# Optimization experiments

Measured on AMD Instinct MI355X. Metric: run time of the kernel, lower is better.

The kernel has to match this reference:

```python
import jax, jax.numpy as jnp
import numpy as np

H = 1024          # en_hidden_size
NUM_LAYERS = 3
NUM_CLASS = 60
IN_SIZE = 150
EPS = 1e-5


def _gru_dir(x, w_ih, w_hh, b_ih, b_hh):
    """Single-direction GRU run forward in time. x: [N,T,in] -> [N,T,H].
    PyTorch GRU cell math."""
    gi = jnp.einsum('nti,gi->ntg', x, w_ih) + b_ih  # [N,T,3H] input projections

    def step(h, gi_t):
        gh = h @ w_hh.T + b_hh
        i_r, i_z, i_n = jnp.split(gi_t, 3, axis=-1)
        h_r, h_z, h_n = jnp.split(gh, 3, axis=-1)
        r = jax.nn.sigmoid(i_r + h_r)
        z = jax.nn.sigmoid(i_z + h_z)
        n = jnp.tanh(i_n + r * h_n)
        h_new = (1.0 - z) * n + z * h
        return h_new, h_new

    h0 = jnp.zeros((x.shape[0], H), dtype=x.dtype)
    _, ys = jax.lax.scan(step, h0, jnp.swapaxes(gi, 0, 1))  # ys: [T,N,H]
    return jnp.swapaxes(ys, 0, 1)


def _bigru_forward(x, bn_gamma, bn_beta,
                   w_ih_0, w_hh_0, b_ih_0, b_hh_0,
                   w_ih_1, w_hh_1, b_ih_1, b_hh_1,
                   w_ih_2, w_hh_2, b_ih_2, b_hh_2,
                   fc_w, fc_b):
    # BatchNorm1d (train mode): stats over (N,T) per channel, biased variance.
    mean = jnp.mean(x, axis=(0, 1), keepdims=True)
    var = jnp.mean(jnp.square(x - mean), axis=(0, 1), keepdims=True)
    h_in = (x - mean) * jax.lax.rsqrt(var + EPS) * bn_gamma + bn_beta

    # NOTE: the original advances the bidirectional GRU one timestep at a time
    # while carrying the hidden state, so BOTH directions run forward in time.
    layer_params = [(w_ih_0, w_hh_0, b_ih_0, b_hh_0),
                    (w_ih_1, w_hh_1, b_ih_1, b_hh_1),
                    (w_ih_2, w_hh_2, b_ih_2, b_hh_2)]
    for (w_ih, w_hh, b_ih, b_hh) in layer_params:
        outs = [_gru_dir(h_in, w_ih[d], w_hh[d], b_ih[d], b_hh[d]) for d in range(2)]
        h_in = jnp.concatenate(outs, axis=-1)  # [N,T,2H]

    encoder_hidden = h_in                      # [N,T,2H]
    hidden = encoder_hidden[:, -1, :]          # seq_len == T for every sample
    out = hidden @ fc_w.T + fc_b               # [N, num_class]
    return out, encoder_hidden


def setup_inputs() -> dict:
    key = jax.random.key(0)
    ks = jax.random.split(key, 32)
    N, T = 256, 64
    s = 1.0 / np.sqrt(H)
    inp = {}
    inp['x'] = jax.random.normal(ks[0], (N, T, IN_SIZE), dtype=jnp.float32)
    inp['bn_gamma'] = jnp.ones((IN_SIZE,), jnp.float32)
    inp['bn_beta'] = jnp.zeros((IN_SIZE,), jnp.float32)
    in_sizes = [IN_SIZE, 2 * H, 2 * H]
    ki = 1
    for l in range(NUM_LAYERS):
        inp[f'w_ih_{l}'] = jax.random.uniform(ks[ki], (2, 3 * H, in_sizes[l]), jnp.float32, -s, s); ki += 1
        inp[f'w_hh_{l}'] = jax.random.uniform(ks[ki], (2, 3 * H, H), jnp.float32, -s, s); ki += 1
        inp[f'b_ih_{l}'] = jax.random.uniform(ks[ki], (2, 3 * H), jnp.float32, -s, s); ki += 1
        inp[f'b_hh_{l}'] = jax.random.uniform(ks[ki], (2, 3 * H), jnp.float32, -s, s); ki += 1
    inp['fc_w'] = jax.random.uniform(ks[ki], (NUM_CLASS, 2 * H), jnp.float32, -s, s); ki += 1
    inp['fc_b'] = jax.random.uniform(ks[ki], (NUM_CLASS,), jnp.float32, -s, s)
    return inp


def reference(x, bn_gamma, bn_beta,
              w_ih_0, w_hh_0, b_ih_0, b_hh_0,
              w_ih_1, w_hh_1, b_ih_1, b_hh_1,
              w_ih_2, w_hh_2, b_ih_2, b_hh_2,
              fc_w, fc_b):
    return _bigru_forward(x, bn_gamma, bn_beta,
                          w_ih_0, w_hh_0, b_ih_0, b_hh_0,
                          w_ih_1, w_hh_1, b_ih_1, b_hh_1,
                          w_ih_2, w_hh_2, b_ih_2, b_hh_2,
                          fc_w, fc_b)
```

## Files before the change

### kernel.cpp

```cpp
#include <hip/hip_runtime.h>
#include <hip/hip_bf16.h>
#include <math.h>

#define HH    1024
#define TT    64
#define NBAT  256
#define G3    3072
#define IN0   150
#define IN0P  160
#define NCLS  60
#define ENC_W 2048

typedef float  f32x4 __attribute__((ext_vector_type(4)));
typedef short  s16x8 __attribute__((ext_vector_type(8)));

#define GLOAD16(gsrc, ldst) \
  __builtin_amdgcn_global_load_lds((const __attribute__((address_space(1))) unsigned int*)(gsrc), \
                                   (__attribute__((address_space(3))) unsigned int*)(ldst), 16, 0, 0)

static __device__ inline short f2bf(float f) {
    __hip_bfloat16 h = __float2bfloat16(f);
    return *(short*)&h;
}

__global__ void bigru_bn_stats(const float* __restrict__ x,
                               float* __restrict__ mean, float* __restrict__ istd) {
    int f = blockIdx.x;
    int tid = threadIdx.x;
    double s = 0.0, s2 = 0.0;
    for (int i = tid; i < NBAT * TT; i += blockDim.x) {
        float v = x[(size_t)i * IN0 + f];
        s += v; s2 += (double)v * v;
    }
    __shared__ double sh[256], sh2[256];
    sh[tid] = s; sh2[tid] = s2;
    __syncthreads();
    for (int off = 128; off > 0; off >>= 1) {
        if (tid < off) { sh[tid] += sh[tid + off]; sh2[tid] += sh2[tid + off]; }
        __syncthreads();
    }
    if (tid == 0) {
        double m = sh[0] / (NBAT * TT);
        double var = sh2[0] / (NBAT * TT) - m * m;
        mean[f] = (float)m;
        istd[f] = (float)(1.0 / sqrt(var + 1e-5));
    }
}

__global__ void bigru_bn_apply_bf16(const float* __restrict__ x,
                                    const float* __restrict__ mean, const float* __restrict__ istd,
                                    const float* __restrict__ gamma, const float* __restrict__ beta,
                                    short* __restrict__ xn) {
    int idx = blockIdx.x * blockDim.x + threadIdx.x;
    if (idx >= NBAT * TT * IN0P) return;
    int f = idx % IN0P;
    int r = idx / IN0P;
    float v = 0.f;
    if (f < IN0) v = (x[(size_t)r * IN0 + f] - mean[f]) * istd[f] * gamma[f] + beta[f];
    xn[idx] = f2bf(v);
}

__global__ void bigru_cvt_wih0(const float* __restrict__ src, short* __restrict__ dst) {
    int idx = blockIdx.x * blockDim.x + threadIdx.x;
    if (idx >= 2 * G3 * IN0P) return;
    int f = idx % IN0P;
    int r = idx / IN0P;
    float v = (f < IN0) ? src[(size_t)r * IN0 + f] : 0.f;
    dst[idx] = f2bf(v);
}

__global__ void bigru_cvt4(const float* __restrict__ src, short* __restrict__ dst, int n4) {
    int i = blockIdx.x * blockDim.x + threadIdx.x;
    if (i >= n4) return;
    float4 v = ((const float4*)src)[i];
    short4 o;
    o.x = f2bf(v.x); o.y = f2bf(v.y); o.z = f2bf(v.z); o.w = f2bf(v.w);
    ((short4*)dst)[i] = o;
}

__global__ __launch_bounds__(256)
void bigru_gi_gemm(const short* __restrict__ Abase, int ldA, int K,
                   const short* __restrict__ W,
                   const float* __restrict__ b_ih,
                   float* __restrict__ gi,
                   int t0, int Mchunk) {
    int d    = blockIdx.z;
    int col0 = blockIdx.x * 128;
    int row0 = blockIdx.y * 128;

    __shared__ short As[128][32];
    __shared__ short Bs[128][32];

    int tid  = threadIdx.x;
    int lane = tid & 63;
    int w    = tid >> 6;
    int wm   = w & 1, wn = w >> 1;

    f32x4 acc[4][4];
    #pragma unroll
    for (int i = 0; i < 4; ++i)
        #pragma unroll
        for (int j = 0; j < 4; ++j)
            acc[i][j] = (f32x4){0.f, 0.f, 0.f, 0.f};

    const short* Wd = W + (size_t)d * G3 * K;
    int sr = lane >> 2;
    int sc = (lane & 3) * 8;

    for (int k0 = 0; k0 < K; k0 += 32) {
        #pragma unroll
        for (int q = 0; q < 2; ++q) {
            int r  = w * 32 + q * 16 + sr;
            int gr = row0 + r;
            int tt = gr >> 8, n = gr & 255;
            const short* ga = Abase + (size_t)(n * TT + t0 + tt) * ldA + k0 + sc;
            GLOAD16(ga, &As[w * 32 + q * 16][0]);
            const short* gb = Wd + (size_t)(col0 + r) * K + k0 + sc;
            GLOAD16(gb, &Bs[w * 32 + q * 16][0]);
        }
        __syncthreads();

        int fr = lane & 15, fq = (lane >> 4) * 8;
        s16x8 a[4], b[4];
        #pragma unroll
        for (int i = 0; i < 4; ++i) a[i] = *(const s16x8*)&As[wm * 64 + i * 16 + fr][fq];
        #pragma unroll
        for (int j = 0; j < 4; ++j) b[j] = *(const s16x8*)&Bs[wn * 64 + j * 16 + fr][fq];
        #pragma unroll
        for (int i = 0; i < 4; ++i)
            #pragma unroll
            for (int j = 0; j < 4; ++j)
                acc[i][j] = __builtin_amdgcn_mfma_f32_16x16x32_bf16(a[i], b[j], acc[i][j], 0, 0, 0);
        __syncthreads();
    }

    int fr = lane & 15, quad = lane >> 4;
    #pragma unroll
    for (int j = 0; j < 4; ++j) {
        int c = col0 + wn * 64 + j * 16 + fr;
        float bias = b_ih[d * G3 + c];
        #pragma unroll
        for (int i = 0; i < 4; ++i) {
            #pragma unroll
            for (int reg = 0; reg < 4; ++reg) {
                int r = row0 + wm * 64 + i * 16 + quad * 4 + reg;
                gi[((size_t)d * Mchunk + r) * G3 + c] = acc[i][j][reg] + bias;
            }
        }
    }
}

__global__ __launch_bounds__(512, 1)
void bigru_steps_fused(const short* __restrict__ w_hh,
                       const float* __restrict__ b_hh,
                       const float* __restrict__ gi,
                       float* __restrict__ h,
                       short* __restrict__ hbf,
                       float* __restrict__ enc,
                       short* __restrict__ enc_bf,
                       unsigned int* __restrict__ bar,
                       int t0, int Tc, int Mchunk) {
    __shared__ short Ws[48 * 1024];
    __shared__ short As[8][4][512];

    int b   = blockIdx.x;
    int d   = b & 1;
    int mt  = (b >> 1) & 1;
    int ct  = b >> 2;
    int grp = b & 3;

    int tid  = threadIdx.x;
    int lane = tid & 63;
    int w    = tid >> 6;
    int fr   = lane & 15;
    int quad = lane >> 4;
    int sw   = fr & 7;

    int j0 = ct * 16;
    int row_base = mt * 128 + w * 16;
    int jcol = j0 + fr;

    const short* Wd = w_hh + (size_t)d * G3 * HH;

    #pragma unroll
    for (int q = 0; q < 12; ++q) {
        int c  = w * 12 + q;
        int rr = c >> 1, kh = c & 1;
        int g  = rr >> 4, jc = rr & 15;
        const short* src = Wd + (size_t)(g * HH + j0 + jc) * HH
                         + (size_t)(kh * 64 + (lane ^ (rr & 7))) * 8;
        GLOAD16(src, &Ws[rr * 1024 + kh * 512]);
    }

    int l0 = lane & 1, l1 = (lane >> 1) & 1, l2 = (lane >> 2) & 1;
    int l3 = (lane >> 3) & 1, l4 = (lane >> 4) & 1, l5 = (lane >> 5) & 1;
    int arow = (l2 ^ l4) | (l3 << 1) | (l4 << 2) | (l5 << 3);
    int akb  = (l0 ^ l2 ^ l4) | ((l1 ^ l3) << 1);
    size_t a_src_off = (size_t)(row_base + arow) * HH + (size_t)akb * 8;

    float hreg[4];
    #pragma unroll
    for (int r = 0; r < 4; ++r) {
        int n = row_base + quad * 4 + r;
        hreg[r] = h[((size_t)d * NBAT + n) * HH + jcol];
    }
    float bhr = b_hh[d * G3 + jcol];
    float bhz = b_hh[d * G3 + HH + jcol];
    float bhn = b_hh[d * G3 + 2 * HH + jcol];

    __syncthreads();

    float gir[4], giz[4], gin[4];
    {
        size_t gb0 = ((size_t)d * Mchunk) * G3 + jcol;
        #pragma unroll
        for (int r = 0; r < 4; ++r) {
            int n = row_base + quad * 4 + r;
            size_t gg = gb0 + (size_t)n * G3;
            gir[r] = gi[gg];
            giz[r] = gi[gg + HH];
            gin[r] = gi[gg + 2 * HH];
        }
    }

    for (int tt = 0; tt < Tc; ++tt) {
        int t = t0 + tt;
        const short* hb = hbf + ((size_t)((t & 1) * 2 + d)) * NBAT * HH;
        short*       ho = hbf + ((size_t)(((t + 1) & 1) * 2 + d)) * NBAT * HH;
        const short* asrc = hb + a_src_off;

        f32x4 acc[3];
        #pragma unroll
        for (int g = 0; g < 3; ++g) acc[g] = (f32x4){0.f, 0.f, 0.f, 0.f};

        #pragma unroll
        for (int c = 0; c < 3; ++c)
            GLOAD16(asrc + c * 32, &As[w][c][0]);

        int rd_off = (fr * 64 + quad * 16) ^ ((fr & 7) << 4);

        #pragma unroll
        for (int c = 0; c < 32; ++c) {
            if (c < 30)       asm volatile("s_waitcnt vmcnt(2)");
            else if (c == 30) asm volatile("s_waitcnt vmcnt(1)");
            else              asm volatile("s_waitcnt vmcnt(0)");
            __builtin_amdgcn_sched_barrier(0);
            s16x8 a = *(const s16x8*)((const char*)&As[w][c & 3][0] + rd_off);
            int ks = c * 4 + quad;
            #pragma unroll
            for (int g = 0; g < 3; ++g) {
                s16x8 bg = *(const s16x8*)&Ws[(g * 16 + fr) * 1024 + ((ks ^ sw) << 3)];
                acc[g] = __builtin_amdgcn_mfma_f32_16x16x32_bf16(a, bg, acc[g], 0, 0, 0);
            }
            __builtin_amdgcn_sched_barrier(0);
            if (c + 3 < 32)
                GLOAD16(asrc + (c + 3) * 32, &As[w][(c + 3) & 3][0]);
        }

        #pragma unroll
        for (int r = 0; r < 4; ++r) {
            int n = row_base + quad * 4 + r;
            float hrv = acc[0][r] + bhr;
            float hzv = acc[1][r] + bhz;
            float hnv = acc[2][r] + bhn;
            float rg = 1.f / (1.f + __expf(-(gir[r] + hrv)));
            float zg = 1.f / (1.f + __expf(-(giz[r] + hzv)));
            float ng = tanhf(gin[r] + rg * hnv);
            float hnew = (1.f - zg) * ng + zg * hreg[r];
            hreg[r] = hnew;
            ho[(size_t)n * HH + jcol] = f2bf(hnew);
            size_t eidx = ((size_t)n * TT + t) * ENC_W + (size_t)d * HH + jcol;
            if (enc_bf) enc_bf[eidx] = f2bf(hnew);
            if (enc)    enc[eidx]    = hnew;
        }

        if (tt == Tc - 1) {
            #pragma unroll
            for (int r = 0; r < 4; ++r) {
                int n = row_base + quad * 4 + r;
                h[((size_t)d * NBAT + n) * HH + jcol] = hreg[r];
            }
        } else {
            size_t gbn = ((size_t)d * Mchunk + (size_t)(tt + 1) * NBAT) * G3 + jcol;
            #pragma unroll
            for (int r = 0; r < 4; ++r) {
                int n = row_base + quad * 4 + r;
                size_t gg = gbn + (size_t)n * G3;
                gir[r] = gi[gg];
                giz[r] = gi[gg + HH];
                gin[r] = gi[gg + 2 * HH];
            }
            __syncthreads();
            if (w == 0) {
                unsigned int* fl = bar + (size_t)grp * 64 * 32;
                unsigned tgt = (unsigned)(tt + 1);
                if (lane == 0)
                    __hip_atomic_store(&fl[ct * 32], tgt,
                                       __ATOMIC_RELEASE, __HIP_MEMORY_SCOPE_AGENT);
                for (;;) {
                    unsigned v = __hip_atomic_load(&fl[lane * 32],
                                                   __ATOMIC_ACQUIRE, __HIP_MEMORY_SCOPE_AGENT);
                    if (__all(v >= tgt)) break;
                    __builtin_amdgcn_s_sleep(2);
                }
            }
            __syncthreads();
        }
    }
}

__global__ void bigru_fc(const float* __restrict__ enc, const float* __restrict__ fc_w,
                         const float* __restrict__ fc_b, float* __restrict__ out) {
    int n = blockIdx.x;
    int tid = threadIdx.x;
    __shared__ float hbuf[ENC_W];
    for (int k = tid; k < ENC_W; k += blockDim.x)
        hbuf[k] = enc[(size_t)n * TT * ENC_W + (size_t)(TT - 1) * ENC_W + k];
    __syncthreads();
    if (tid < NCLS) {
        float acc = fc_b[tid];
        for (int k = 0; k < ENC_W; ++k)
            acc += hbuf[k] * fc_w[(size_t)tid * ENC_W + k];
        out[(size_t)n * NCLS + tid] = acc;
    }
}

extern "C" void kernel_launch(void* const* d_in, const int* in_sizes, int n_in,
                              void* d_out, int out_size, void* d_ws, size_t ws_size,
                              hipStream_t stream) {
    const float* x        = (const float*)d_in[0];
    const float* bn_gamma = (const float*)d_in[1];
    const float* bn_beta  = (const float*)d_in[2];
    const float* w_ih[3]  = {(const float*)d_in[3], (const float*)d_in[7],  (const float*)d_in[11]};
    const float* w_hh[3]  = {(const float*)d_in[4], (const float*)d_in[8],  (const float*)d_in[12]};
    const float* b_ih[3]  = {(const float*)d_in[5], (const float*)d_in[9],  (const float*)d_in[13]};
    const float* b_hh[3]  = {(const float*)d_in[6], (const float*)d_in[10], (const float*)d_in[14]};
    const float* fc_w     = (const float*)d_in[15];
    const float* fc_b     = (const float*)d_in[16];

    float* out = (float*)d_out;
    float* enc = out + NBAT * NCLS;

    char* base = (char*)d_ws;
    size_t off = 0;
    auto alloc = [&](size_t bytes) {
        void* p = base + off;
        off += (bytes + 255) & ~(size_t)255;
        return p;
    };
    float* mean      = (float*)alloc(IN0 * 4);
    float* istd      = (float*)alloc(IN0 * 4);
    short* xn_bf     = (short*)alloc((size_t)NBAT * TT * IN0P * 2);
    short* wih0_bf   = (short*)alloc((size_t)2 * G3 * IN0P * 2);
    short* wih_bf    = (short*)alloc((size_t)2 * G3 * ENC_W * 2);
    short* whh_bf    = (short*)alloc((size_t)2 * G3 * HH * 2);
    float* h         = (float*)alloc((size_t)2 * NBAT * HH * 4);
    short* hbf       = (short*)alloc((size_t)2 * 2 * NBAT * HH * 2);
    short* enc_bf    = (short*)alloc((size_t)NBAT * TT * ENC_W * 2);
    unsigned int* bar = (unsigned int*)alloc((size_t)4 * 64 * 32 * sizeof(unsigned int));
    size_t fixed = off;

    int Tc = 1;
    for (int cand : {16, 8, 4, 2, 1}) {
        size_t gi_bytes = (size_t)2 * NBAT * cand * G3 * 4;
        if (fixed + gi_bytes + 1024 <= ws_size) { Tc = cand; break; }
    }
    float* gi = (float*)alloc((size_t)2 * NBAT * Tc * G3 * 4);
    int Mchunk = NBAT * Tc;

    bigru_bn_stats<<<IN0, 256, 0, stream>>>(x, mean, istd);
    bigru_bn_apply_bf16<<<(NBAT * TT * IN0P + 255) / 256, 256, 0, stream>>>(
        x, mean, istd, bn_gamma, bn_beta, xn_bf);

    bigru_cvt_wih0<<<(2 * G3 * IN0P + 255) / 256, 256, 0, stream>>>(w_ih[0], wih0_bf);

    for (int l = 0; l < 3; ++l) {
        if (l > 0) {
            int n4 = (2 * G3 * ENC_W) / 4;
            bigru_cvt4<<<(n4 + 255) / 256, 256, 0, stream>>>(w_ih[l], wih_bf, n4);
        }
        {
            int n4 = (2 * G3 * HH) / 4;
            bigru_cvt4<<<(n4 + 255) / 256, 256, 0, stream>>>(w_hh[l], whh_bf, n4);
        }
        hipMemsetAsync(h, 0, (size_t)2 * NBAT * HH * 4, stream);
        hipMemsetAsync(hbf, 0, (size_t)2 * 2 * NBAT * HH * 2, stream);

        const short* Abase = (l == 0) ? xn_bf : enc_bf;
        int ldA = (l == 0) ? IN0P : ENC_W;
        int K   = (l == 0) ? IN0P : ENC_W;
        const short* W = (l == 0) ? wih0_bf : wih_bf;

        for (int t0 = 0; t0 < TT; t0 += Tc) {
            bigru_gi_gemm<<<dim3(G3 / 128, Mchunk / 128, 2), 256, 0, stream>>>(
                Abase, ldA, K, W, b_ih[l], gi, t0, Mchunk);

            hipMemsetAsync(bar, 0, (size_t)4 * 64 * 32 * sizeof(unsigned int), stream);

            const short* whh_c   = whh_bf;
            const float* bhh_c   = b_hh[l];
            const float* gi_c    = gi;
            float*       h_c     = h;
            short*       hbf_c   = hbf;
            float*       enc_c   = (l == 2) ? enc : nullptr;
            short*       encbf_c = (l == 2) ? nullptr : enc_bf;
            unsigned int* bar_c  = bar;
            int a_t0 = t0, a_tc = Tc, a_mc = Mchunk;
            void* kargs[] = { &whh_c, &bhh_c, &gi_c, &h_c, &hbf_c,
                              &enc_c, &encbf_c, &bar_c, &a_t0, &a_tc, &a_mc };
            hipLaunchCooperativeKernel((const void*)bigru_steps_fused,
                                       dim3(256), dim3(512), kargs, 0, stream);
        }
    }

    bigru_fc<<<NBAT, 256, 0, stream>>>(enc, fc_w, fc_b, out);
}
```

Before: 4.867 ms.

## Store gi in fp16 and halve step-kernel waves with two row tiles each

The input-projection GEMM now writes gi as fp16 instead of fp32, halving its memory traffic and workspace footprint, which may also permit a larger time chunk. The recurrent step kernel drops from 512 to 256 threads per block, with each wave computing two 16-row tiles that share the same W_hh fragments, doubling MFMA work per wave and loads in flight. This trades wave-level parallelism for instruction-level parallelism and reuse of LDS weight reads, and adds fp16 rounding of gi.

```diff
diff --git a/kernel.cpp b/kernel.cpp
--- a/kernel.cpp
+++ b/kernel.cpp
@@ -1,5 +1,6 @@
 #include <hip/hip_runtime.h>
 #include <hip/hip_bf16.h>
+#include <hip/hip_fp16.h>
 #include <math.h>
 
 #define HH    1024
@@ -82,7 +83,7 @@
 void bigru_gi_gemm(const short* __restrict__ Abase, int ldA, int K,
                    const short* __restrict__ W,
                    const float* __restrict__ b_ih,
-                   float* __restrict__ gi,
+                   __half* __restrict__ gi,
                    int t0, int Mchunk) {
     int d    = blockIdx.z;
     int col0 = blockIdx.x * 128;
@@ -144,16 +145,16 @@
             #pragma unroll
             for (int reg = 0; reg < 4; ++reg) {
                 int r = row0 + wm * 64 + i * 16 + quad * 4 + reg;
-                gi[((size_t)d * Mchunk + r) * G3 + c] = acc[i][j][reg] + bias;
-            }
-        }
-    }
-}
-
-__global__ __launch_bounds__(512, 1)
+                gi[((size_t)d * Mchunk + r) * G3 + c] = __float2half(acc[i][j][reg] + bias);
+            }
+        }
+    }
+}
+
+__global__ __launch_bounds__(256, 1)
 void bigru_steps_fused(const short* __restrict__ w_hh,
                        const float* __restrict__ b_hh,
-                       const float* __restrict__ gi,
+                       const __half* __restrict__ gi,
                        float* __restrict__ h,
                        short* __restrict__ hbf,
                        float* __restrict__ enc,
@@ -161,7 +162,7 @@
                        unsigned int* __restrict__ bar,
                        int t0, int Tc, int Mchunk) {
     __shared__ short Ws[48 * 1024];
-    __shared__ short As[8][4][512];
+    __shared__ short As[4][4][1024];
 
     int b   = blockIdx.x;
     int d   = b & 1;
@@ -177,14 +178,14 @@
     int sw   = fr & 7;
 
     int j0 = ct * 16;
-    int row_base = mt * 128 + w * 16;
+    int row_base = mt * 128 + w * 32;
     int jcol = j0 + fr;
 
     const short* Wd = w_hh + (size_t)d * G3 * HH;
 
     #pragma unroll
-    for (int q = 0; q < 12; ++q) {
-        int c  = w * 12 + q;
+    for (int q = 0; q < 24; ++q) {
+        int c  = w * 24 + q;
         int rr = c >> 1, kh = c & 1;
         int g  = rr >> 4, jc = rr & 15;
         const short* src = Wd + (size_t)(g * HH + j0 + jc) * HH
@@ -196,100 +197,123 @@
     int l3 = (lane >> 3) & 1, l4 = (lane >> 4) & 1, l5 = (lane >> 5) & 1;
     int arow = (l2 ^ l4) | (l3 << 1) | (l4 << 2) | (l5 << 3);
     int akb  = (l0 ^ l2 ^ l4) | ((l1 ^ l3) << 1);
-    size_t a_src_off = (size_t)(row_base + arow) * HH + (size_t)akb * 8;
-
-    float hreg[4];
+    size_t a_src0 = (size_t)(row_base + arow) * HH + (size_t)akb * 8;
+    size_t a_src1 = (size_t)(row_base + 16 + arow) * HH + (size_t)akb * 8;
+
+    float hreg[2][4];
     #pragma unroll
-    for (int r = 0; r < 4; ++r) {
-        int n = row_base + quad * 4 + r;
-        hreg[r] = h[((size_t)d * NBAT + n) * HH + jcol];
-    }
+    for (int hh = 0; hh < 2; ++hh)
+        #pragma unroll
+        for (int r = 0; r < 4; ++r) {
+            int n = row_base + hh * 16 + quad * 4 + r;
+            hreg[hh][r] = h[((size_t)d * NBAT + n) * HH + jcol];
+        }
     float bhr = b_hh[d * G3 + jcol];
     float bhz = b_hh[d * G3 + HH + jcol];
     float bhn = b_hh[d * G3 + 2 * HH + jcol];
 
     __syncthreads();
 
-    float gir[4], giz[4], gin[4];
+    float gir[2][4], giz[2][4], gin[2][4];
     {
         size_t gb0 = ((size_t)d * Mchunk) * G3 + jcol;
         #pragma unroll
-        for (int r = 0; r < 4; ++r) {
-            int n = row_base + quad * 4 + r;
-            size_t gg = gb0 + (size_t)n * G3;
-            gir[r] = gi[gg];
-            giz[r] = gi[gg + HH];
-            gin[r] = gi[gg + 2 * HH];
-        }
+        for (int hh = 0; hh < 2; ++hh)
+            #pragma unroll
+            for (int r = 0; r < 4; ++r) {
+                int n = row_base + hh * 16 + quad * 4 + r;
+                size_t gg = gb0 + (size_t)n * G3;
+                gir[hh][r] = __half2float(gi[gg]);
+                giz[hh][r] = __half2float(gi[gg + HH]);
+                gin[hh][r] = __half2float(gi[gg + 2 * HH]);
+            }
     }
 
     for (int tt = 0; tt < Tc; ++tt) {
         int t = t0 + tt;
         const short* hb = hbf + ((size_t)((t & 1) * 2 + d)) * NBAT * HH;
         short*       ho = hbf + ((size_t)(((t + 1) & 1) * 2 + d)) * NBAT * HH;
-        const short* asrc = hb + a_src_off;
-
-        f32x4 acc[3];
-        #pragma unroll
-        for (int g = 0; g < 3; ++g) acc[g] = (f32x4){0.f, 0.f, 0.f, 0.f};
-
-        #pragma unroll
-        for (int c = 0; c < 3; ++c)
-            GLOAD16(asrc + c * 32, &As[w][c][0]);
+        const short* asrc0 = hb + a_src0;
+        const short* asrc1 = hb + a_src1;
+
+        f32x4 acc[2][3];
+        #pragma unroll
+        for (int hh = 0; hh < 2; ++hh)
+            #pragma unroll
+            for (int g = 0; g < 3; ++g)
+                acc[hh][g] = (f32x4){0.f, 0.f, 0.f, 0.f};
+
+        #pragma unroll
+        for (int c = 0; c < 3; ++c) {
+            GLOAD16(asrc0 + c * 32, &As[w][c][0]);
+            GLOAD16(asrc1 + c * 32, &As[w][c][512]);
+        }
 
         int rd_off = (fr * 64 + quad * 16) ^ ((fr & 7) << 4);
 
         #pragma unroll
         for (int c = 0; c < 32; ++c) {
-            if (c < 30)       asm volatile("s_waitcnt vmcnt(2)");
-            else if (c == 30) asm volatile("s_waitcnt vmcnt(1)");
+            if (c < 30)       asm volatile("s_waitcnt vmcnt(4)");
+            else if (c == 30) asm volatile("s_waitcnt vmcnt(2)");
             else              asm volatile("s_waitcnt vmcnt(0)");
             __builtin_amdgcn_sched_barrier(0);
-            s16x8 a = *(const s16x8*)((const char*)&As[w][c & 3][0] + rd_off);
+            const char* slot = (const char*)&As[w][c & 3][0];
+            s16x8 a0 = *(const s16x8*)(slot + rd_off);
+            s16x8 a1 = *(const s16x8*)(slot + 1024 + rd_off);
             int ks = c * 4 + quad;
             #pragma unroll
             for (int g = 0; g < 3; ++g) {
                 s16x8 bg = *(const s16x8*)&Ws[(g * 16 + fr) * 1024 + ((ks ^ sw) << 3)];
-                acc[g] = __builtin_amdgcn_mfma_f32_16x16x32_bf16(a, bg, acc[g], 0, 0, 0);
+                acc[0][g] = __builtin_amdgcn_mfma_f32_16x16x32_bf16(a0, bg, acc[0][g], 0, 0, 0);
+                acc[1][g] = __builtin_amdgcn_mfma_f32_16x16x32_bf16(a1, bg, acc[1][g], 0, 0, 0);
             }
             __builtin_amdgcn_sched_barrier(0);
-            if (c + 3 < 32)
-                GLOAD16(asrc + (c + 3) * 32, &As[w][(c + 3) & 3][0]);
-        }
-
-        #pragma unroll
-        for (int r = 0; r < 4; ++r) {
-            int n = row_base + quad * 4 + r;
-            float hrv = acc[0][r] + bhr;
-            float hzv = acc[1][r] + bhz;
-            float hnv = acc[2][r] + bhn;
-            float rg = 1.f / (1.f + __expf(-(gir[r] + hrv)));
-            float zg = 1.f / (1.f + __expf(-(giz[r] + hzv)));
-            float ng = tanhf(gin[r] + rg * hnv);
-            float hnew = (1.f - zg) * ng + zg * hreg[r];
-            hreg[r] = hnew;
-            ho[(size_t)n * HH + jcol] = f2bf(hnew);
-            size_t eidx = ((size_t)n * TT + t) * ENC_W + (size_t)d * HH + jcol;
-            if (enc_bf) enc_bf[eidx] = f2bf(hnew);
-            if (enc)    enc[eidx]    = hnew;
+            if (c + 3 < 32) {
+                GLOAD16(asrc0 + (c + 3) * 32, &As[w][(c + 3) & 3][0]);
+                GLOAD16(asrc1 + (c + 3) * 32, &As[w][(c + 3) & 3][512]);
+            }
+        }
+
+        #pragma unroll
+        for (int hh = 0; hh < 2; ++hh) {
+            #pragma unroll
+            for (int r = 0; r < 4; ++r) {
+                int n = row_base + hh * 16 + quad * 4 + r;
+                float hrv = acc[hh][0][r] + bhr;
+                float hzv = acc[hh][1][r] + bhz;
+                float hnv = acc[hh][2][r] + bhn;
+                float rg = 1.f / (1.f + __expf(-(gir[hh][r] + hrv)));
+                float zg = 1.f / (1.f + __expf(-(giz[hh][r] + hzv)));
+                float ng = tanhf(gin[hh][r] + rg * hnv);
+                float hnew = (1.f - zg) * ng + zg * hreg[hh][r];
+                hreg[hh][r] = hnew;
+                ho[(size_t)n * HH + jcol] = f2bf(hnew);
+                size_t eidx = ((size_t)n * TT + t) * ENC_W + (size_t)d * HH + jcol;
+                if (enc_bf) enc_bf[eidx] = f2bf(hnew);
+                if (enc)    enc[eidx]    = hnew;
+            }
         }
 
         if (tt == Tc - 1) {
             #pragma unroll
-            for (int r = 0; r < 4; ++r) {
-                int n = row_base + quad * 4 + r;
-                h[((size_t)d * NBAT + n) * HH + jcol] = hreg[r];
-            }
+            for (int hh = 0; hh < 2; ++hh)
+                #pragma unroll
+                for (int r = 0; r < 4; ++r) {
+                    int n = row_base + hh * 16 + quad * 4 + r;
+                    h[((size_t)d * NBAT + n) * HH + jcol] = hreg[hh][r];
+                }
         } else {
             size_t gbn = ((size_t)d * Mchunk + (size_t)(tt + 1) * NBAT) * G3 + jcol;
             #pragma unroll
-            for (int r = 0; r < 4; ++r) {
-                int n = row_base + quad * 4 + r;
-                size_t gg = gbn + (size_t)n * G3;
-                gir[r] = gi[gg];
-                giz[r] = gi[gg + HH];
-                gin[r] = gi[gg + 2 * HH];
-            }
+            for (int hh = 0; hh < 2; ++hh)
+                #pragma unroll
+                for (int r = 0; r < 4; ++r) {
+                    int n = row_base + hh * 16 + quad * 4 + r;
+                    size_t gg = gbn + (size_t)n * G3;
+                    gir[hh][r] = __half2float(gi[gg]);
+                    giz[hh][r] = __half2float(gi[gg + HH]);
+                    gin[hh][r] = __half2float(gi[gg + 2 * HH]);
+                }
             __syncthreads();
             if (w == 0) {
                 unsigned int* fl = bar + (size_t)grp * 64 * 32;
@@ -362,10 +386,10 @@
 
     int Tc = 1;
     for (int cand : {16, 8, 4, 2, 1}) {
-        size_t gi_bytes = (size_t)2 * NBAT * cand * G3 * 4;
+        size_t gi_bytes = (size_t)2 * NBAT * cand * G3 * 2;
         if (fixed + gi_bytes + 1024 <= ws_size) { Tc = cand; break; }
     }
-    float* gi = (float*)alloc((size_t)2 * NBAT * Tc * G3 * 4);
+    __half* gi = (__half*)alloc((size_t)2 * NBAT * Tc * G3 * 2);
     int Mchunk = NBAT * Tc;
 
     bigru_bn_stats<<<IN0, 256, 0, stream>>>(x, mean, istd);
@@ -399,7 +423,7 @@
 
             const short* whh_c   = whh_bf;
             const float* bhh_c   = b_hh[l];
-            const float* gi_c    = gi;
+            const __half* gi_c   = gi;
             float*       h_c     = h;
             short*       hbf_c   = hbf;
             float*       enc_c   = (l == 2) ? enc : nullptr;
@@ -409,7 +433,7 @@
             void* kargs[] = { &whh_c, &bhh_c, &gi_c, &h_c, &hbf_c,
                               &enc_c, &encbf_c, &bar_c, &a_t0, &a_tc, &a_mc };
             hipLaunchCooperativeKernel((const void*)bigru_steps_fused,
-                                       dim3(256), dim3(512), kargs, 0, stream);
+                                       dim3(256), dim3(256), kargs, 0, stream);
         }
     }
 
```

New measurement: 4.879 ms. No clear change (+0.3%).
